# Optimization experiments

Hardware: AMD Instinct MI355X
Metric: run time of the kernel (lower is better)

## Reference

```python
import jax, jax.numpy as jnp
import numpy as np
from jax import lax

B_, DIM, H, W, Dd = 2, 256, 16, 16, 16
DI, N, DTR, K = 256, 8, 16, 4   # d_inner (expand=1), d_state, dt_rank=ceil(256/16), d_conv
OUT_C = 1200
L = H * W * Dd
EPS = 1e-5


def setup_inputs() -> dict:
    key = jax.random.key(0)
    ks = jax.random.split(key, 20)
    g = lambda k, s: jax.random.normal(k, s, jnp.float32) * 0.02
    A_log = jnp.log(jnp.broadcast_to(jnp.arange(1, N + 1, dtype=jnp.float32), (DI, N)))
    dt_bias = jnp.full((DI,), float(np.log(np.expm1(0.01))), jnp.float32)
    return {
        "input0": jax.random.normal(ks[0], (B_, DIM, H, W, Dd), jnp.float32),
        "input1": jax.random.normal(ks[1], (B_, DIM, H, W, Dd), jnp.float32),
        "norm0_w": jnp.ones((DIM,), jnp.float32),
        "norm0_b": jnp.zeros((DIM,), jnp.float32),
        "norm1_w": jnp.ones((DIM,), jnp.float32),
        "norm1_b": jnp.zeros((DIM,), jnp.float32),
        "in_proj_w": g(ks[2], (DI, DIM)),
        "in_projz_w": g(ks[3], (DI, DIM)),
        "conv1d_w": g(ks[4], (DI, 1, K)),
        "conv1d_bias": jnp.zeros((DI,), jnp.float32),
        "conv1db_w": g(ks[5], (DI, 1, K)),
        "conv1db_bias": jnp.zeros((DI,), jnp.float32),
        "xproj_w": g(ks[6], (DTR + 2 * N, DI)),
        "xprojb_w": g(ks[7], (DTR + 2 * N, DI)),
        "dtproj_w": g(ks[8], (DI, DTR)),
        "dtproj_bias": dt_bias,
        "dtprojb_w": g(ks[9], (DI, DTR)),
        "dtprojb_bias": dt_bias,
        "A_log": A_log,
        "Ab_log": A_log,
        "D_p": jnp.ones((DI,), jnp.float32),
        "D_b": jnp.ones((DI,), jnp.float32),
        "rms_w": jnp.ones((DI,), jnp.float32),
        "out_proj_w": g(ks[10], (DIM, DI)),
        "conv3d_w": g(ks[11], (OUT_C, DIM)),
        "conv3d_bias": jnp.zeros((OUT_C,), jnp.float32),
    }


def _layernorm(x, w, b):
    m = x.mean(-1, keepdims=True)
    v = ((x - m) ** 2).mean(-1, keepdims=True)
    return (x - m) * lax.rsqrt(v + EPS) * w + b


def _rmsnorm(x, w):
    return x * lax.rsqrt((x * x).mean(-1, keepdims=True) + EPS) * w


def _ssm_dir(x, z, conv_w, conv_b, xproj_w, dtproj_w, dtproj_bias, A_log, Dp):
    # One direction of the bimamba-v2 selective scan. x, z: (b, L, d_inner)
    xt = x.transpose(0, 2, 1)  # (b, d, L)
    xc = lax.conv_general_dilated(xt, conv_w, (1,), [(K - 1, 0)], feature_group_count=DI)
    x = jax.nn.silu(xc + conv_b[None, :, None]).transpose(0, 2, 1)  # causal dw-conv + silu
    dbl = x @ xproj_w.T                                   # (b, L, dt_rank + 2n)
    dt, Bm, Cm = dbl[..., :DTR], dbl[..., DTR:DTR + N], dbl[..., DTR + N:]
    dt = jax.nn.softplus(dt @ dtproj_w.T + dtproj_bias)    # (b, L, d)
    A = -jnp.exp(A_log)                                    # (d, n)
    dA = jnp.exp(dt[..., None] * A)                        # (b, L, d, n)
    dBu = (dt * x)[..., None] * Bm[:, :, None, :]          # (b, L, d, n)

    def step(h, inp):
        dA_t, dBu_t, C_t = inp
        h = h * dA_t + dBu_t
        return h, jnp.einsum('bdn,bn->bd', h, C_t)

    h0 = jnp.zeros((x.shape[0], DI, N), x.dtype)
    _, ys = lax.scan(step, h0, (dA.transpose(1, 0, 2, 3), dBu.transpose(1, 0, 2, 3), Cm.transpose(1, 0, 2)))
    y = ys.transpose(1, 0, 2) + x * Dp                     # (b, L, d)
    return y * jax.nn.silu(z)                              # gate from the matching branch


def _forward(input0, input1, norm0_w, norm0_b, norm1_w, norm1_b, in_proj_w, in_projz_w,
             conv1d_w, conv1d_bias, conv1db_w, conv1db_bias, xproj_w, xprojb_w,
             dtproj_w, dtproj_bias, dtprojb_w, dtprojb_bias, A_log, Ab_log,
             D_p, D_b, rms_w, out_proj_w, conv3d_w, conv3d_bias):
    b = input0.shape[0]
    skip = input0
    seq0 = input0.transpose(0, 2, 3, 4, 1).reshape(b, L, DIM)  # b (h w d) c
    seq1 = input1.transpose(0, 2, 3, 4, 1).reshape(b, L, DIM)
    seq0 = _layernorm(seq0, norm0_w, norm0_b)
    seq1 = _layernorm(seq1, norm1_w, norm1_b)
    x = seq0 @ in_proj_w.T    # SSM input from input0
    z = seq1 @ in_projz_w.T   # gate from extra_emb (input1)
    y_f = _ssm_dir(x, z, conv1d_w, conv1d_bias, xproj_w, dtproj_w, dtproj_bias, A_log, D_p)
    y_b = _ssm_dir(x[:, ::-1], z[:, ::-1], conv1db_w, conv1db_bias, xprojb_w,
                   dtprojb_w, dtprojb_bias, Ab_log, D_b)[:, ::-1]

    def head(y):
        o = _rmsnorm(y, rms_w) @ out_proj_w.T              # use_norm=True, then out_proj
        o = o.reshape(b, H, W, Dd, DIM).transpose(0, 4, 1, 2, 3) + skip
        return jnp.einsum('bchwd,oc->bohwd', o, conv3d_w) + conv3d_bias[None, :, None, None, None]

    out = head((y_f + y_b) * 0.5)   # if_devide_out=True
    return out, head(y_f), head(y_b)


def reference(input0, input1, norm0_w, norm0_b, norm1_w, norm1_b, in_proj_w, in_projz_w,
              conv1d_w, conv1d_bias, conv1db_w, conv1db_bias, xproj_w, xprojb_w,
              dtproj_w, dtproj_bias, dtprojb_w, dtprojb_bias, A_log, Ab_log,
              D_p, D_b, rms_w, out_proj_w, conv3d_w, conv3d_bias):
    return _forward(input0, input1, norm0_w, norm0_b, norm1_w, norm1_b, in_proj_w, in_projz_w,
                    conv1d_w, conv1d_bias, conv1db_w, conv1db_bias, xproj_w, xprojb_w,
                    dtproj_w, dtproj_bias, dtprojb_w, dtprojb_bias, A_log, Ab_log,
                    D_p, D_b, rms_w, out_proj_w, conv3d_w, conv3d_bias)
```

## Files before the change

kernel.cpp:

```cpp
#include <hip/hip_runtime.h>
#include <cstdint>

#define NTOK 8192

typedef __attribute__((ext_vector_type(4))) float f32x4;
typedef __attribute__((ext_vector_type(8))) short s16x8;

__device__ __forceinline__ short f2bf(float f) {
  union { float f; unsigned u; } x; x.f = f;
  unsigned r = x.u + 0x7FFFu + ((x.u >> 16) & 1u);
  return (short)(r >> 16);
}
__device__ __forceinline__ float bf2f(short s) {
  union { float f; unsigned u; } x;
  x.u = ((unsigned)(unsigned short)s) << 16;
  return x.f;
}
__device__ __forceinline__ void gl_lds16(const void* g, void* l) {
  __builtin_amdgcn_global_load_lds((const unsigned int*)g, (unsigned int*)l, 16, 0, 0);
}

__global__ __launch_bounds__(256) void ln_transpose_kernel(
    const float* __restrict__ in0, const float* __restrict__ in1,
    const float* __restrict__ w0, const float* __restrict__ b0,
    const float* __restrict__ w1, const float* __restrict__ b1,
    const float* __restrict__ wxp, const float* __restrict__ wzp,
    const float* __restrict__ wop, const float* __restrict__ wcp,
    short* __restrict__ Wx, short* __restrict__ Wz,
    short* __restrict__ Wo, short* __restrict__ Wc,
    short* __restrict__ xlnz, float* __restrict__ seqT)
{
  __shared__ float tile[32 * 257];
  __shared__ float mu[32], rs[32];
  const int tid = threadIdx.x;
  const int b  = blockIdx.x >> 7;
  const int l0 = (blockIdx.x & 127) << 5;

  {
    int base = (int)blockIdx.x << 11;
    #pragma unroll
    for (int i = 0; i < 8; ++i) {
      int idx = base + (i << 8) + tid;
      if (idx < 65536)       Wx[idx] = f2bf(wxp[idx]);
      else if (idx < 131072) Wz[idx - 65536] = f2bf(wzp[idx - 65536]);
      else if (idx < 196608) Wo[idx - 131072] = f2bf(wop[idx - 131072]);
      else {
        int k = idx - 196608;
        Wc[k] = ((k >> 8) < 1200) ? f2bf(wcp[k]) : (short)0;
      }
    }
  }

  for (int pass = 0; pass < 2; ++pass) {
    const float* in = pass ? in1 : in0;
    #pragma unroll 8
    for (int i = 0; i < 32; ++i) {
      int e = (i << 8) + tid;
      int c = e >> 5, lo = e & 31;
      tile[lo * 257 + c] = in[((size_t)(b * 256 + c) << 12) + l0 + lo];
    }
    __syncthreads();
    if (tid < 64) {
      int r = tid & 31, h = tid >> 5;
      float s = 0.f, ss = 0.f;
      #pragma unroll 16
      for (int c = h * 128; c < h * 128 + 128; ++c) {
        float v = tile[r * 257 + c];
        s += v; ss += v * v;
      }
      s  += __shfl_xor(s, 32, 64);
      ss += __shfl_xor(ss, 32, 64);
      if (h == 0) {
        float m = s * (1.f / 256.f);
        mu[r] = m;
        rs[r] = rsqrtf(ss * (1.f / 256.f) - m * m + 1e-5f);
      }
    }
    __syncthreads();
    const float* w  = pass ? w1 : w0;
    const float* bb = pass ? b1 : b0;
    float wv = w[tid], bv = bb[tid];
    #pragma unroll 8
    for (int i = 0; i < 32; ++i) {
      float v = tile[i * 257 + tid];
      int row = (pass ? 8192 : 0) + (b << 12) + l0 + i;
      xlnz[(size_t)row * 256 + tid] = f2bf((v - mu[i]) * rs[i] * wv + bv);
      if (pass == 0) seqT[(((size_t)b << 12) + l0 + i) * 256 + tid] = v;
    }
    __syncthreads();
  }
}

template <int EPI>
__global__ __launch_bounds__(256) void gemm_fast(
    const short* __restrict__ A, const short* __restrict__ W0,
    const short* __restrict__ W1, float* __restrict__ Cf,
    short* __restrict__ Cb, const float* __restrict__ ADD,
    const float* __restrict__ bias, int Msplit)
{
  __shared__ short As[4096];
  __shared__ short Bs[4096];
  const int tid  = threadIdx.x;
  const int lane = tid & 63, wave = tid >> 6;
  const int m0 = blockIdx.y << 7;
  const int n0 = blockIdx.x << 7;
  const short* W = (EPI == 0 && m0 >= Msplit) ? W1 : W0;

  const int sr = tid >> 2;
  const int sc = (tid & 3) << 3;
  const int mf = lane & 15, kq = lane >> 4;
  const int wm = (wave & 1) << 6, wn = (wave >> 1) << 6;

  const short* Ar0 = A + (size_t)(m0 + sr) * 256 + sc;
  const short* Ar1 = A + (size_t)(m0 + 64 + sr) * 256 + sc;
  const short* Br0 = W + (size_t)(n0 + sr) * 256 + sc;
  const short* Br1 = W + (size_t)(n0 + 64 + sr) * 256 + sc;
  short* AsW = &As[wave << 9];
  short* BsW = &Bs[wave << 9];

  f32x4 acc[4][4] = {};

  for (int kt = 0; kt < 256; kt += 32) {
    gl_lds16(Ar0 + kt, AsW);
    gl_lds16(Ar1 + kt, AsW + 2048);
    gl_lds16(Br0 + kt, BsW);
    gl_lds16(Br1 + kt, BsW + 2048);
    __syncthreads();
    s16x8 af[4], bfr[4];
    #pragma unroll
    for (int i = 0; i < 4; ++i)
      af[i] = *(const s16x8*)&As[((wm + (i << 4) + mf) << 5) + (kq << 3)];
    #pragma unroll
    for (int j = 0; j < 4; ++j)
      bfr[j] = *(const s16x8*)&Bs[((wn + (j << 4) + mf) << 5) + (kq << 3)];
    #pragma unroll
    for (int i = 0; i < 4; ++i)
      #pragma unroll
      for (int j = 0; j < 4; ++j)
        acc[i][j] = __builtin_amdgcn_mfma_f32_16x16x32_bf16(af[i], bfr[j], acc[i][j], 0, 0, 0);
    __syncthreads();
  }

  if (EPI == 0) {
    #pragma unroll
    for (int i = 0; i < 4; ++i) {
      int gm = m0 + wm + (i << 4) + (kq << 2);
      #pragma unroll
      for (int j = 0; j < 4; ++j) {
        int gn = n0 + wn + (j << 4) + mf;
        #pragma unroll
        for (int r = 0; r < 4; ++r)
          Cf[(size_t)(gm + r) * 256 + gn] = acc[i][j][r];
      }
    }
  } else if (EPI == 1) {
    #pragma unroll
    for (int i = 0; i < 4; ++i) {
      int gm = m0 + wm + (i << 4) + (kq << 2);
      #pragma unroll
      for (int j = 0; j < 4; ++j) {
        int gn = n0 + wn + (j << 4) + mf;
        #pragma unroll
        for (int r = 0; r < 4; ++r) {
          int tok = (gm + r) & 8191;
          float v = acc[i][j][r] + ADD[(size_t)tok * 256 + gn];
          Cb[(size_t)(gm + r) * 256 + gn] = f2bf(v);
        }
      }
    }
  } else {
    const int head = m0 >> 13, bb = (m0 >> 12) & 1, lb = m0 & 4095;
    float* obase = Cf + (size_t)head * (2u * 1200u * 4096u) + (size_t)bb * (1200u * 4096u);
    #pragma unroll
    for (int i = 0; i < 4; ++i) {
      int l = lb + wm + (i << 4) + (kq << 2);
      #pragma unroll
      for (int j = 0; j < 4; ++j) {
        int gn = n0 + wn + (j << 4) + mf;
        if (gn < 1200) {
          float bv = bias[gn];
          f32x4 v = acc[i][j];
          v[0] += bv; v[1] += bv; v[2] += bv; v[3] += bv;
          __builtin_nontemporal_store(v, (f32x4*)&obase[(size_t)gn * 4096 + l]);
        }
      }
    }
  }
}

__global__ __launch_bounds__(256) void fused_front(
    const float* __restrict__ x,
    const float* __restrict__ cw0, const float* __restrict__ cb0,
    const float* __restrict__ cw1, const float* __restrict__ cb1,
    const float* __restrict__ xw0, const float* __restrict__ xw1,
    const float* __restrict__ dtw0, const float* __restrict__ dtb0,
    const float* __restrict__ dtw1, const float* __restrict__ dtb1,
    const float* __restrict__ Alog0, const float* __restrict__ Alog1,
    float* __restrict__ xcg, float* __restrict__ dblg,
    float* __restrict__ P, float* __restrict__ Q)
{
  __shared__ float xcs[16 * 256];
  __shared__ short wxs[256 * 33];
  __shared__ float dls[512];
  const int tid = threadIdx.x;
  const int dir = blockIdx.x >> 9;
  const int b   = (blockIdx.x >> 8) & 1;
  const int ch  = blockIdx.x & 255;
  const int t0  = ch << 4;
  const float* cw   = dir ? cw1 : cw0;
  const float* cb   = dir ? cb1 : cb0;
  const float* xw   = dir ? xw1 : xw0;
  const float* dtw  = dir ? dtw1 : dtw0;
  const float* dtb  = dir ? dtb1 : dtb0;
  const float* Alog = dir ? Alog1 : Alog0;
  const size_t dS = (size_t)dir * (NTOK * 256);
  const size_t xb = ((size_t)b) << 12;

  {
    const int d = tid;
    const float w0 = cw[(d << 2)], w1 = cw[(d << 2) + 1],
                w2 = cw[(d << 2) + 2], w3 = cw[(d << 2) + 3];
    const float bias = cb[d];
    float h0 = 0.f, h1 = 0.f, h2 = 0.f;
    #pragma unroll
    for (int i = 0; i < 3; ++i) {
      int ts = t0 - 3 + i; float v = 0.f;
      if (ts >= 0) { int tn = dir ? 4095 - ts : ts; v = x[(xb + tn) * 256 + d]; }
      h0 = h1; h1 = h2; h2 = v;
    }
    #pragma unroll
    for (int s = 0; s < 16; ++s) {
      int ts = t0 + s;
      int tn = dir ? 4095 - ts : ts;
      float xv = x[(xb + tn) * 256 + d];
      float a = bias + w0 * h0 + w1 * h1 + w2 * h2 + w3 * xv;
      h0 = h1; h1 = h2; h2 = xv;
      float v = a / (1.f + __expf(-a));
      xcs[s * 256 + d] = v;
      xcg[dS + (xb + ts) * 256 + d] = v;
    }
  }
  #pragma unroll
  for (int i = 0; i < 32; ++i) {
    int flat = (i << 8) + tid;
    wxs[(flat & 255) * 33 + (flat >> 8)] = f2bf(xw[flat]);
  }
  __syncthreads();

  {
    const int j = tid & 31, s0 = tid >> 5;
    float a0 = 0.f, a1 = 0.f;
    #pragma unroll 8
    for (int r = 0; r < 256; ++r) {
      float w = bf2f(wxs[r * 33 + j]);
      a0 = fmaf(xcs[s0 * 256 + r], w, a0);
      a1 = fmaf(xcs[(s0 + 8) * 256 + r], w, a1);
    }
    dls[(s0 << 5) + j] = a0;
    dls[((s0 + 8) << 5) + j] = a1;
    size_t db = (size_t)dir * 262144 + ((xb + t0) << 5);
    dblg[db + tid] = a0;
    dblg[db + 256 + tid] = a1;
  }
  __syncthreads();

  {
    const int d = tid;
    float wrow[16];
    #pragma unroll
    for (int r = 0; r < 16; ++r) wrow[r] = dtw[(d << 4) + r];
    const float bias = dtb[d];
    float Av[8], p[8], q[8];
    #pragma unroll
    for (int n = 0; n < 8; ++n) {
      Av[n] = -expf(Alog[(d << 3) + n]); p[n] = 1.f; q[n] = 0.f;
    }
    for (int s = 0; s < 16; ++s) {
      float a = bias;
      #pragma unroll
      for (int r = 0; r < 16; ++r) a = fmaf(dls[(s << 5) + r], wrow[r], a);
      float dtv = (a > 20.f) ? a : log1pf(__expf(a));
      float xv = xcs[s * 256 + d];
      float du = dtv * xv;
      #pragma unroll
      for (int n = 0; n < 8; ++n) {
        float dA = __expf(dtv * Av[n]);
        p[n] *= dA;
        q[n] = fmaf(q[n], dA, du * dls[(s << 5) + 16 + n]);
      }
    }
    size_t ob = (size_t)dir * 1048576 + ((size_t)((b << 8) + ch) * 8) * 256 + d;
    #pragma unroll
    for (int n = 0; n < 8; ++n) { P[ob + (n << 8)] = p[n]; Q[ob + (n << 8)] = q[n]; }
  }
}

__global__ __launch_bounds__(256) void scan_p2(
    const float* __restrict__ P, const float* __restrict__ Q, float* __restrict__ Hs)
{
  const int d = threadIdx.x;
  const int bid = blockIdx.x;
  const int dir = bid >> 4, b = (bid >> 3) & 1, n = bid & 7;
  const size_t dOff = (size_t)dir * 1048576;
  float h = 0.f;
  #pragma unroll 8
  for (int ch = 0; ch < 256; ++ch) {
    size_t i = dOff + ((size_t)((b << 8) + ch) * 8 + n) * 256 + d;
    Hs[i] = h;
    h = fmaf(P[i], h, Q[i]);
  }
}

__global__ __launch_bounds__(256) void scan_p3(
    const float* __restrict__ xcg, const float* __restrict__ dblg,
    const float* __restrict__ dtw0, const float* __restrict__ dtb0,
    const float* __restrict__ dtw1, const float* __restrict__ dtb1,
    const float* __restrict__ Hs, const float* __restrict__ z,
    const float* __restrict__ Alog0, const float* __restrict__ Alog1,
    const float* __restrict__ Dp0, const float* __restrict__ Dp1,
    short* __restrict__ yall)
{
  __shared__ float dl[512];
  const int d = threadIdx.x;
  const int dir = blockIdx.x >> 9;
  const int b   = (blockIdx.x >> 8) & 1;
  const int ch  = blockIdx.x & 255;
  const int t0  = ch << 4;
  const float* dtw  = dir ? dtw1 : dtw0;
  const float* dtb  = dir ? dtb1 : dtb0;
  const float* Alog = dir ? Alog1 : Alog0;
  const float* Dp   = dir ? Dp1 : Dp0;
  const size_t dS = (size_t)dir * (NTOK * 256);
  const size_t xb = ((size_t)b) << 12;
  short* y = yall + (size_t)dir * (NTOK * 256);

  size_t db = (size_t)dir * 262144 + ((xb + t0) << 5);
  dl[d]       = dblg[db + d];
  dl[256 + d] = dblg[db + 256 + d];
  float wrow[16];
  #pragma unroll
  for (int r = 0; r < 16; ++r) wrow[r] = dtw[(d << 4) + r];
  const float bias = dtb[d];
  float Av[8], h[8];
  #pragma unroll
  for (int n = 0; n < 8; ++n) Av[n] = -expf(Alog[(d << 3) + n]);
  size_t hb = (size_t)dir * 1048576 + ((size_t)((b << 8) + ch) * 8) * 256 + d;
  #pragma unroll
  for (int n = 0; n < 8; ++n) h[n] = Hs[hb + (n << 8)];
  const float Dv = Dp[d];
  __syncthreads();
  for (int s = 0; s < 16; ++s) {
    float a = bias;
    #pragma unroll
    for (int r = 0; r < 16; ++r) a = fmaf(dl[(s << 5) + r], wrow[r], a);
    float dtv = (a > 20.f) ? a : log1pf(__expf(a));
    int ts = t0 + s;
    float xv = xcg[dS + (xb + ts) * 256 + d];
    float du = dtv * xv;
    float yv = 0.f;
    #pragma unroll
    for (int n = 0; n < 8; ++n) {
      float dA = __expf(dtv * Av[n]);
      h[n] = fmaf(h[n], dA, du * dl[(s << 5) + 16 + n]);
      yv = fmaf(h[n], dl[(s << 5) + 24 + n], yv);
    }
    yv = fmaf(xv, Dv, yv);
    int tn = dir ? (4095 - ts) : ts;
    size_t zi = (xb + tn) * 256 + d;
    float zv = z[zi];
    y[zi] = f2bf(yv * zv / (1.f + __expf(-zv)));
  }
}

__global__ __launch_bounds__(256) void rms_all(
    const short* __restrict__ yf, const short* __restrict__ yb,
    const float* __restrict__ w, short* __restrict__ yn)
{
  const int d = threadIdx.x;
  const int mode = blockIdx.y;
  const size_t tok = blockIdx.x;
  size_t i = tok * 256 + d;
  float v;
  if (mode == 0)      v = 0.5f * (bf2f(yf[i]) + bf2f(yb[i]));
  else if (mode == 1) v = bf2f(yf[i]);
  else                v = bf2f(yb[i]);
  float ss = v * v;
  #pragma unroll
  for (int o = 32; o > 0; o >>= 1) ss += __shfl_xor(ss, o, 64);
  __shared__ float red[4];
  if ((d & 63) == 0) red[d >> 6] = ss;
  __syncthreads();
  float tot = red[0] + red[1] + red[2] + red[3];
  float sc = rsqrtf(tot * (1.f / 256.f) + 1e-5f);
  yn[((size_t)mode * 8192 + tok) * 256 + d] = f2bf(v * sc * w[d]);
}

extern "C" void kernel_launch(void* const* d_in, const int* in_sizes, int n_in,
                              void* d_out, int out_size, void* d_ws, size_t ws_size,
                              hipStream_t stream) {
  const float* in0        = (const float*)d_in[0];
  const float* in1        = (const float*)d_in[1];
  const float* n0w        = (const float*)d_in[2];
  const float* n0b        = (const float*)d_in[3];
  const float* n1w        = (const float*)d_in[4];
  const float* n1b        = (const float*)d_in[5];
  const float* in_proj_w  = (const float*)d_in[6];
  const float* in_projz_w = (const float*)d_in[7];
  const float* conv1d_w   = (const float*)d_in[8];
  const float* conv1d_b   = (const float*)d_in[9];
  const float* conv1db_w  = (const float*)d_in[10];
  const float* conv1db_b  = (const float*)d_in[11];
  const float* xproj_w    = (const float*)d_in[12];
  const float* xprojb_w   = (const float*)d_in[13];
  const float* dtproj_w   = (const float*)d_in[14];
  const float* dtproj_b   = (const float*)d_in[15];
  const float* dtprojb_w  = (const float*)d_in[16];
  const float* dtprojb_b  = (const float*)d_in[17];
  const float* A_log      = (const float*)d_in[18];
  const float* Ab_log     = (const float*)d_in[19];
  const float* D_p        = (const float*)d_in[20];
  const float* D_b        = (const float*)d_in[21];
  const float* rms_w      = (const float*)d_in[22];
  const float* out_proj_w = (const float*)d_in[23];
  const float* conv3d_w   = (const float*)d_in[24];
  const float* conv3d_b   = (const float*)d_in[25];
  (void)in_sizes; (void)n_in; (void)out_size; (void)ws_size;

  float* ws = (float*)d_ws;
  size_t o = 0;
  short* xlnz = (short*)(ws + o); o += 2097152;
  float* seqT = ws + o;           o += 2097152;
  float* x    = ws + o;           o += 2097152;
  float* z    = ws + o;           o += 2097152;
  float* xc2  = ws + o;           o += 4194304;
  float* dbl2 = ws + o;           o += 524288;
  float* P    = ws + o;           o += 2097152;
  float* Q    = ws + o;           o += 2097152;
  float* Hs   = ws + o;           o += 2097152;
  short* yall = (short*)(ws + o); o += 2097152;
  short* yn   = (short*)(ws + o); o += 3145728;
  short* obuf = (short*)(ws + o); o += 3145728;
  short* Wx   = (short*)(ws + o); o += 32768;
  short* Wz   = (short*)(ws + o); o += 32768;
  short* Wo   = (short*)(ws + o); o += 32768;
  short* Wc   = (short*)(ws + o); o += 163840;
  float* out  = (float*)d_out;

  dim3 blk(256);

  ln_transpose_kernel<<<dim3(256), blk, 0, stream>>>(
      in0, in1, n0w, n0b, n1w, n1b,
      in_proj_w, in_projz_w, out_proj_w, conv3d_w, Wx, Wz, Wo, Wc,
      xlnz, seqT);

  gemm_fast<0><<<dim3(2, 128), blk, 0, stream>>>(xlnz, Wx, Wz, x, nullptr, nullptr, nullptr, 8192);

  fused_front<<<dim3(1024), blk, 0, stream>>>(
      x, conv1d_w, conv1d_b, conv1db_w, conv1db_b,
      xproj_w, xprojb_w, dtproj_w, dtproj_b, dtprojb_w, dtprojb_b,
      A_log, Ab_log, xc2, dbl2, P, Q);

  scan_p2<<<dim3(32), blk, 0, stream>>>(P, Q, Hs);

  scan_p3<<<dim3(1024), blk, 0, stream>>>(
      xc2, dbl2, dtproj_w, dtproj_b, dtprojb_w, dtprojb_b,
      Hs, z, A_log, Ab_log, D_p, D_b, yall);

  rms_all<<<dim3(8192, 3), blk, 0, stream>>>(yall, yall + 2097152, rms_w, yn);
  gemm_fast<1><<<dim3(2, 192), blk, 0, stream>>>(yn, Wo, nullptr, nullptr, obuf, seqT, nullptr, 0);
  gemm_fast<2><<<dim3(10, 192), blk, 0, stream>>>(obuf, Wc, nullptr, out, nullptr, nullptr, conv3d_b, 0);
}
```

Before: 339.0 us.

## Split SSM front into conv, MFMA x_proj GEMM, and hierarchical chunk scan

Replaces the fused_front kernel, which did the x_proj projection as a scalar LDS dot product per block, with three stages. A bf16 conv+SiLU kernel is followed by a small MFMA GEMM for the 32-wide x_proj output, with the weights pre-converted to bf16 in the setup kernel. The conv+SiLU is recomputed in scan_p1 and scan_p3 instead of storing and reloading fp32 xc, and those kernels read dbl straight from global memory. The serial 256-step inter-chunk scan (32 blocks) becomes a two-level scan over 512 blocks each, adding launches and redundant conv work in exchange for more parallelism and tensor-core use.

```diff
diff --git a/kernel.cpp b/kernel.cpp
--- a/kernel.cpp
+++ b/kernel.cpp
@@ -26,8 +26,9 @@
     const float* __restrict__ w1, const float* __restrict__ b1,
     const float* __restrict__ wxp, const float* __restrict__ wzp,
     const float* __restrict__ wop, const float* __restrict__ wcp,
+    const float* __restrict__ xwf, const float* __restrict__ xwb,
     short* __restrict__ Wx, short* __restrict__ Wz,
-    short* __restrict__ Wo, short* __restrict__ Wc,
+    short* __restrict__ Wo, short* __restrict__ Wc, short* __restrict__ Wxp,
     short* __restrict__ xlnz, float* __restrict__ seqT)
 {
   __shared__ float tile[32 * 257];
@@ -36,18 +37,17 @@
   const int b  = blockIdx.x >> 7;
   const int l0 = (blockIdx.x & 127) << 5;
 
-  {
-    int base = (int)blockIdx.x << 11;
-    #pragma unroll
-    for (int i = 0; i < 8; ++i) {
-      int idx = base + (i << 8) + tid;
-      if (idx < 65536)       Wx[idx] = f2bf(wxp[idx]);
-      else if (idx < 131072) Wz[idx - 65536] = f2bf(wzp[idx - 65536]);
-      else if (idx < 196608) Wo[idx - 131072] = f2bf(wop[idx - 131072]);
-      else {
-        int k = idx - 196608;
-        Wc[k] = ((k >> 8) < 1200) ? f2bf(wcp[k]) : (short)0;
-      }
+  for (int idx = (int)blockIdx.x * 256 + tid; idx < 540672; idx += 65536) {
+    if (idx < 65536)       Wx[idx] = f2bf(wxp[idx]);
+    else if (idx < 131072) Wz[idx - 65536] = f2bf(wzp[idx - 65536]);
+    else if (idx < 196608) Wo[idx - 131072] = f2bf(wop[idx - 131072]);
+    else if (idx < 524288) {
+      int k = idx - 196608;
+      Wc[k] = ((k >> 8) < 1200) ? f2bf(wcp[k]) : (short)0;
+    } else {
+      int k = idx - 524288;
+      int j = k & 8191;
+      Wxp[k] = f2bf((k >> 13) ? xwb[j] : xwf[j]);
     }
   }
 
@@ -188,36 +188,91 @@
   }
 }
 
-__global__ __launch_bounds__(256) void fused_front(
+__global__ __launch_bounds__(256) void conv_silu_b(
     const float* __restrict__ x,
     const float* __restrict__ cw0, const float* __restrict__ cb0,
     const float* __restrict__ cw1, const float* __restrict__ cb1,
-    const float* __restrict__ xw0, const float* __restrict__ xw1,
+    short* __restrict__ xcb)
+{
+  const int d = threadIdx.x;
+  const int dir = blockIdx.x >> 9;
+  const int b   = (blockIdx.x >> 8) & 1;
+  const int t0  = (blockIdx.x & 255) << 4;
+  const float* cw = dir ? cw1 : cw0;
+  const float* cb = dir ? cb1 : cb0;
+  const float w0 = cw[(d << 2)], w1 = cw[(d << 2) + 1],
+              w2 = cw[(d << 2) + 2], w3 = cw[(d << 2) + 3];
+  const float bias = cb[d];
+  const size_t xb = ((size_t)b) << 12;
+  short* orow = xcb + ((size_t)(dir << 13) + (b << 12) + t0) * 256 + d;
+  float h0 = 0.f, h1 = 0.f, h2 = 0.f;
+  #pragma unroll
+  for (int i = 0; i < 3; ++i) {
+    int ts = t0 - 3 + i; float v = 0.f;
+    if (ts >= 0) { int tn = dir ? 4095 - ts : ts; v = x[(xb + tn) * 256 + d]; }
+    h0 = h1; h1 = h2; h2 = v;
+  }
+  #pragma unroll
+  for (int s = 0; s < 16; ++s) {
+    int tn = dir ? 4095 - (t0 + s) : (t0 + s);
+    float xv = x[(xb + tn) * 256 + d];
+    float a = bias + w0 * h0 + w1 * h1 + w2 * h2 + w3 * xv;
+    h0 = h1; h1 = h2; h2 = xv;
+    orow[(size_t)s * 256] = f2bf(a / (1.f + __expf(-a)));
+  }
+}
+
+__global__ __launch_bounds__(256) void gemm_n32(
+    const short* __restrict__ A, const short* __restrict__ Wxp,
+    float* __restrict__ Cdbl)
+{
+  const int lane = threadIdx.x & 63, wave = threadIdx.x >> 6;
+  const int mf = lane & 15, kq = lane >> 4;
+  const int m0 = ((int)blockIdx.x << 6) + (wave << 4);
+  const short* W = Wxp + ((m0 >= 8192) ? 8192 : 0);
+  const short* Arow = A + (size_t)(m0 + mf) * 256 + (kq << 3);
+  const short* B0 = W + (size_t)mf * 256 + (kq << 3);
+  const short* B1 = W + (size_t)(16 + mf) * 256 + (kq << 3);
+  f32x4 acc[2] = {};
+  #pragma unroll
+  for (int kt = 0; kt < 256; kt += 32) {
+    s16x8 af = *(const s16x8*)(Arow + kt);
+    s16x8 b0 = *(const s16x8*)(B0 + kt);
+    s16x8 b1 = *(const s16x8*)(B1 + kt);
+    acc[0] = __builtin_amdgcn_mfma_f32_16x16x32_bf16(af, b0, acc[0], 0, 0, 0);
+    acc[1] = __builtin_amdgcn_mfma_f32_16x16x32_bf16(af, b1, acc[1], 0, 0, 0);
+  }
+  #pragma unroll
+  for (int j = 0; j < 2; ++j)
+    #pragma unroll
+    for (int r = 0; r < 4; ++r)
+      Cdbl[(size_t)(m0 + (kq << 2) + r) * 32 + (j << 4) + mf] = acc[j][r];
+}
+
+__global__ __launch_bounds__(256) void scan_p1(
+    const float* __restrict__ x,
+    const float* __restrict__ cw0, const float* __restrict__ cb0,
+    const float* __restrict__ cw1, const float* __restrict__ cb1,
+    const float* __restrict__ dbl,
     const float* __restrict__ dtw0, const float* __restrict__ dtb0,
     const float* __restrict__ dtw1, const float* __restrict__ dtb1,
-    const float* __restrict__ Alog0, const float* __restrict__ Alog1,
-    float* __restrict__ xcg, float* __restrict__ dblg,
+    const float* __restrict__ Al0, const float* __restrict__ Al1,
     float* __restrict__ P, float* __restrict__ Q)
 {
-  __shared__ float xcs[16 * 256];
-  __shared__ short wxs[256 * 33];
-  __shared__ float dls[512];
-  const int tid = threadIdx.x;
+  const int d = threadIdx.x;
   const int dir = blockIdx.x >> 9;
   const int b   = (blockIdx.x >> 8) & 1;
   const int ch  = blockIdx.x & 255;
   const int t0  = ch << 4;
   const float* cw   = dir ? cw1 : cw0;
   const float* cb   = dir ? cb1 : cb0;
-  const float* xw   = dir ? xw1 : xw0;
   const float* dtw  = dir ? dtw1 : dtw0;
   const float* dtb  = dir ? dtb1 : dtb0;
-  const float* Alog = dir ? Alog1 : Alog0;
-  const size_t dS = (size_t)dir * (NTOK * 256);
+  const float* Alog = dir ? Al1 : Al0;
   const size_t xb = ((size_t)b) << 12;
 
+  float xc[16];
   {
-    const int d = tid;
     const float w0 = cw[(d << 2)], w1 = cw[(d << 2) + 1],
                 w2 = cw[(d << 2) + 2], w3 = cw[(d << 2) + 3];
     const float bias = cb[d];
@@ -230,141 +285,162 @@
     }
     #pragma unroll
     for (int s = 0; s < 16; ++s) {
-      int ts = t0 + s;
-      int tn = dir ? 4095 - ts : ts;
+      int tn = dir ? 4095 - (t0 + s) : (t0 + s);
       float xv = x[(xb + tn) * 256 + d];
       float a = bias + w0 * h0 + w1 * h1 + w2 * h2 + w3 * xv;
       h0 = h1; h1 = h2; h2 = xv;
-      float v = a / (1.f + __expf(-a));
-      xcs[s * 256 + d] = v;
-      xcg[dS + (xb + ts) * 256 + d] = v;
-    }
-  }
-  #pragma unroll
-  for (int i = 0; i < 32; ++i) {
-    int flat = (i << 8) + tid;
-    wxs[(flat & 255) * 33 + (flat >> 8)] = f2bf(xw[flat]);
-  }
-  __syncthreads();
-
-  {
-    const int j = tid & 31, s0 = tid >> 5;
-    float a0 = 0.f, a1 = 0.f;
-    #pragma unroll 8
-    for (int r = 0; r < 256; ++r) {
-      float w = bf2f(wxs[r * 33 + j]);
-      a0 = fmaf(xcs[s0 * 256 + r], w, a0);
-      a1 = fmaf(xcs[(s0 + 8) * 256 + r], w, a1);
-    }
-    dls[(s0 << 5) + j] = a0;
-    dls[((s0 + 8) << 5) + j] = a1;
-    size_t db = (size_t)dir * 262144 + ((xb + t0) << 5);
-    dblg[db + tid] = a0;
-    dblg[db + 256 + tid] = a1;
-  }
-  __syncthreads();
-
-  {
-    const int d = tid;
-    float wrow[16];
-    #pragma unroll
-    for (int r = 0; r < 16; ++r) wrow[r] = dtw[(d << 4) + r];
-    const float bias = dtb[d];
-    float Av[8], p[8], q[8];
+      xc[s] = a / (1.f + __expf(-a));
+    }
+  }
+
+  float wrow[16];
+  #pragma unroll
+  for (int r = 0; r < 16; ++r) wrow[r] = dtw[(d << 4) + r];
+  const float bias_dt = dtb[d];
+  float Av[8], p[8], q[8];
+  #pragma unroll
+  for (int n = 0; n < 8; ++n) {
+    Av[n] = -expf(Alog[(d << 3) + n]); p[n] = 1.f; q[n] = 0.f;
+  }
+  const float* drow = dbl + ((size_t)(dir << 13) + (b << 12) + t0) * 32;
+  #pragma unroll 4
+  for (int s = 0; s < 16; ++s) {
+    float a = bias_dt;
+    #pragma unroll
+    for (int r = 0; r < 16; ++r) a = fmaf(drow[(s << 5) + r], wrow[r], a);
+    float dtv = (a > 20.f) ? a : log1pf(__expf(a));
+    float du = dtv * xc[s];
     #pragma unroll
     for (int n = 0; n < 8; ++n) {
-      Av[n] = -expf(Alog[(d << 3) + n]); p[n] = 1.f; q[n] = 0.f;
-    }
-    for (int s = 0; s < 16; ++s) {
-      float a = bias;
-      #pragma unroll
-      for (int r = 0; r < 16; ++r) a = fmaf(dls[(s << 5) + r], wrow[r], a);
-      float dtv = (a > 20.f) ? a : log1pf(__expf(a));
-      float xv = xcs[s * 256 + d];
-      float du = dtv * xv;
-      #pragma unroll
-      for (int n = 0; n < 8; ++n) {
-        float dA = __expf(dtv * Av[n]);
-        p[n] *= dA;
-        q[n] = fmaf(q[n], dA, du * dls[(s << 5) + 16 + n]);
-      }
-    }
-    size_t ob = (size_t)dir * 1048576 + ((size_t)((b << 8) + ch) * 8) * 256 + d;
-    #pragma unroll
-    for (int n = 0; n < 8; ++n) { P[ob + (n << 8)] = p[n]; Q[ob + (n << 8)] = q[n]; }
-  }
-}
-
-__global__ __launch_bounds__(256) void scan_p2(
-    const float* __restrict__ P, const float* __restrict__ Q, float* __restrict__ Hs)
+      float dA = __expf(dtv * Av[n]);
+      p[n] *= dA;
+      q[n] = fmaf(q[n], dA, du * drow[(s << 5) + 16 + n]);
+    }
+  }
+  size_t ob = (size_t)dir * 1048576 + ((size_t)((b << 8) + ch) << 11) + d;
+  #pragma unroll
+  for (int n = 0; n < 8; ++n) { P[ob + (n << 8)] = p[n]; Q[ob + (n << 8)] = q[n]; }
+}
+
+__global__ __launch_bounds__(256) void scan_p2a(
+    const float* __restrict__ P, const float* __restrict__ Q,
+    float* __restrict__ SP, float* __restrict__ SQ)
 {
   const int d = threadIdx.x;
   const int bid = blockIdx.x;
-  const int dir = bid >> 4, b = (bid >> 3) & 1, n = bid & 7;
-  const size_t dOff = (size_t)dir * 1048576;
+  const int dir = bid >> 8, b = (bid >> 7) & 1, n = (bid >> 4) & 7, sup = bid & 15;
+  float sp = 1.f, sq = 0.f;
+  #pragma unroll 4
+  for (int c = 0; c < 16; ++c) {
+    int ch = (sup << 4) + c;
+    size_t i = (size_t)dir * 1048576 + ((size_t)((b << 8) + ch) << 11) + (n << 8) + d;
+    float pp = P[i], qq = Q[i];
+    sq = fmaf(pp, sq, qq);
+    sp *= pp;
+  }
+  size_t o2 = ((size_t)((((dir << 1) + b) << 3) + n) << 12) + ((size_t)sup << 8) + d;
+  SP[o2] = sp; SQ[o2] = sq;
+}
+
+__global__ __launch_bounds__(256) void scan_p2bc(
+    const float* __restrict__ P, const float* __restrict__ Q,
+    const float* __restrict__ SP, const float* __restrict__ SQ,
+    float* __restrict__ Hs)
+{
+  const int d = threadIdx.x;
+  const int bid = blockIdx.x;
+  const int dir = bid >> 8, b = (bid >> 7) & 1, n = (bid >> 4) & 7, sup = bid & 15;
+  size_t sb = ((size_t)((((dir << 1) + b) << 3) + n) << 12) + d;
   float h = 0.f;
-  #pragma unroll 8
-  for (int ch = 0; ch < 256; ++ch) {
-    size_t i = dOff + ((size_t)((b << 8) + ch) * 8 + n) * 256 + d;
+  for (int s2 = 0; s2 < sup; ++s2) {
+    size_t i = sb + ((size_t)s2 << 8);
+    h = fmaf(SP[i], h, SQ[i]);
+  }
+  #pragma unroll 4
+  for (int c = 0; c < 16; ++c) {
+    int ch = (sup << 4) + c;
+    size_t i = (size_t)dir * 1048576 + ((size_t)((b << 8) + ch) << 11) + (n << 8) + d;
     Hs[i] = h;
     h = fmaf(P[i], h, Q[i]);
   }
 }
 
 __global__ __launch_bounds__(256) void scan_p3(
-    const float* __restrict__ xcg, const float* __restrict__ dblg,
+    const float* __restrict__ x,
+    const float* __restrict__ cw0, const float* __restrict__ cb0,
+    const float* __restrict__ cw1, const float* __restrict__ cb1,
+    const float* __restrict__ dbl,
     const float* __restrict__ dtw0, const float* __restrict__ dtb0,
     const float* __restrict__ dtw1, const float* __restrict__ dtb1,
     const float* __restrict__ Hs, const float* __restrict__ z,
-    const float* __restrict__ Alog0, const float* __restrict__ Alog1,
+    const float* __restrict__ Al0, const float* __restrict__ Al1,
     const float* __restrict__ Dp0, const float* __restrict__ Dp1,
     short* __restrict__ yall)
 {
-  __shared__ float dl[512];
   const int d = threadIdx.x;
   const int dir = blockIdx.x >> 9;
   const int b   = (blockIdx.x >> 8) & 1;
   const int ch  = blockIdx.x & 255;
   const int t0  = ch << 4;
+  const float* cw   = dir ? cw1 : cw0;
+  const float* cb   = dir ? cb1 : cb0;
   const float* dtw  = dir ? dtw1 : dtw0;
   const float* dtb  = dir ? dtb1 : dtb0;
-  const float* Alog = dir ? Alog1 : Alog0;
+  const float* Alog = dir ? Al1 : Al0;
   const float* Dp   = dir ? Dp1 : Dp0;
-  const size_t dS = (size_t)dir * (NTOK * 256);
   const size_t xb = ((size_t)b) << 12;
   short* y = yall + (size_t)dir * (NTOK * 256);
 
-  size_t db = (size_t)dir * 262144 + ((xb + t0) << 5);
-  dl[d]       = dblg[db + d];
-  dl[256 + d] = dblg[db + 256 + d];
+  float xc[16];
+  {
+    const float w0 = cw[(d << 2)], w1 = cw[(d << 2) + 1],
+                w2 = cw[(d << 2) + 2], w3 = cw[(d << 2) + 3];
+    const float bias = cb[d];
+    float h0 = 0.f, h1 = 0.f, h2 = 0.f;
+    #pragma unroll
+    for (int i = 0; i < 3; ++i) {
+      int ts = t0 - 3 + i; float v = 0.f;
+      if (ts >= 0) { int tn = dir ? 4095 - ts : ts; v = x[(xb + tn) * 256 + d]; }
+      h0 = h1; h1 = h2; h2 = v;
+    }
+    #pragma unroll
+    for (int s = 0; s < 16; ++s) {
+      int tn = dir ? 4095 - (t0 + s) : (t0 + s);
+      float xv = x[(xb + tn) * 256 + d];
+      float a = bias + w0 * h0 + w1 * h1 + w2 * h2 + w3 * xv;
+      h0 = h1; h1 = h2; h2 = xv;
+      xc[s] = a / (1.f + __expf(-a));
+    }
+  }
+
   float wrow[16];
   #pragma unroll
   for (int r = 0; r < 16; ++r) wrow[r] = dtw[(d << 4) + r];
-  const float bias = dtb[d];
+  const float bias_dt = dtb[d];
   float Av[8], h[8];
   #pragma unroll
   for (int n = 0; n < 8; ++n) Av[n] = -expf(Alog[(d << 3) + n]);
-  size_t hb = (size_t)dir * 1048576 + ((size_t)((b << 8) + ch) * 8) * 256 + d;
+  size_t hb = (size_t)dir * 1048576 + ((size_t)((b << 8) + ch) << 11) + d;
   #pragma unroll
   for (int n = 0; n < 8; ++n) h[n] = Hs[hb + (n << 8)];
   const float Dv = Dp[d];
-  __syncthreads();
+  const float* drow = dbl + ((size_t)(dir << 13) + (b << 12) + t0) * 32;
+  #pragma unroll 4
   for (int s = 0; s < 16; ++s) {
-    float a = bias;
-    #pragma unroll
-    for (int r = 0; r < 16; ++r) a = fmaf(dl[(s << 5) + r], wrow[r], a);
+    float a = bias_dt;
+    #pragma unroll
+    for (int r = 0; r < 16; ++r) a = fmaf(drow[(s << 5) + r], wrow[r], a);
     float dtv = (a > 20.f) ? a : log1pf(__expf(a));
-    int ts = t0 + s;
-    float xv = xcg[dS + (xb + ts) * 256 + d];
-    float du = dtv * xv;
+    float du = dtv * xc[s];
     float yv = 0.f;
     #pragma unroll
     for (int n = 0; n < 8; ++n) {
       float dA = __expf(dtv * Av[n]);
-      h[n] = fmaf(h[n], dA, du * dl[(s << 5) + 16 + n]);
-      yv = fmaf(h[n], dl[(s << 5) + 24 + n], yv);
-    }
-    yv = fmaf(xv, Dv, yv);
+      h[n] = fmaf(h[n], dA, du * drow[(s << 5) + 16 + n]);
+      yv = fmaf(h[n], drow[(s << 5) + 24 + n], yv);
+    }
+    yv = fmaf(xc[s], Dv, yv);
+    int ts = t0 + s;
     int tn = dir ? (4095 - ts) : ts;
     size_t zi = (xb + tn) * 256 + d;
     float zv = z[zi];
@@ -432,11 +508,13 @@
   float* seqT = ws + o;           o += 2097152;
   float* x    = ws + o;           o += 2097152;
   float* z    = ws + o;           o += 2097152;
-  float* xc2  = ws + o;           o += 4194304;
-  float* dbl2 = ws + o;           o += 524288;
+  short* xcb  = (short*)(ws + o); o += 2097152;
+  float* dbl  = ws + o;           o += 524288;
   float* P    = ws + o;           o += 2097152;
   float* Q    = ws + o;           o += 2097152;
   float* Hs   = ws + o;           o += 2097152;
+  float* SP   = ws + o;           o += 131072;
+  float* SQ   = ws + o;           o += 131072;
   short* yall = (short*)(ws + o); o += 2097152;
   short* yn   = (short*)(ws + o); o += 3145728;
   short* obuf = (short*)(ws + o); o += 3145728;
@@ -444,27 +522,33 @@
   short* Wz   = (short*)(ws + o); o += 32768;
   short* Wo   = (short*)(ws + o); o += 32768;
   short* Wc   = (short*)(ws + o); o += 163840;
+  short* Wxp  = (short*)(ws + o); o += 8192;
   float* out  = (float*)d_out;
 
   dim3 blk(256);
 
   ln_transpose_kernel<<<dim3(256), blk, 0, stream>>>(
       in0, in1, n0w, n0b, n1w, n1b,
-      in_proj_w, in_projz_w, out_proj_w, conv3d_w, Wx, Wz, Wo, Wc,
-      xlnz, seqT);
+      in_proj_w, in_projz_w, out_proj_w, conv3d_w, xproj_w, xprojb_w,
+      Wx, Wz, Wo, Wc, Wxp, xlnz, seqT);
 
   gemm_fast<0><<<dim3(2, 128), blk, 0, stream>>>(xlnz, Wx, Wz, x, nullptr, nullptr, nullptr, 8192);
 
-  fused_front<<<dim3(1024), blk, 0, stream>>>(
-      x, conv1d_w, conv1d_b, conv1db_w, conv1db_b,
-      xproj_w, xprojb_w, dtproj_w, dtproj_b, dtprojb_w, dtprojb_b,
-      A_log, Ab_log, xc2, dbl2, P, Q);
-
-  scan_p2<<<dim3(32), blk, 0, stream>>>(P, Q, Hs);
+  conv_silu_b<<<dim3(1024), blk, 0, stream>>>(x, conv1d_w, conv1d_b, conv1db_w, conv1db_b, xcb);
+
+  gemm_n32<<<dim3(256), blk, 0, stream>>>(xcb, Wxp, dbl);
+
+  scan_p1<<<dim3(1024), blk, 0, stream>>>(
+      x, conv1d_w, conv1d_b, conv1db_w, conv1db_b, dbl,
+      dtproj_w, dtproj_b, dtprojb_w, dtprojb_b, A_log, Ab_log, P, Q);
+
+  scan_p2a<<<dim3(512), blk, 0, stream>>>(P, Q, SP, SQ);
+  scan_p2bc<<<dim3(512), blk, 0, stream>>>(P, Q, SP, SQ, Hs);
 
   scan_p3<<<dim3(1024), blk, 0, stream>>>(
-      xc2, dbl2, dtproj_w, dtproj_b, dtprojb_w, dtprojb_b,
-      Hs, z, A_log, Ab_log, D_p, D_b, yall);
+      x, conv1d_w, conv1d_b, conv1db_w, conv1db_b, dbl,
+      dtproj_w, dtproj_b, dtprojb_w, dtprojb_b, Hs, z,
+      A_log, Ab_log, D_p, D_b, yall);
 
   rms_all<<<dim3(8192, 3), blk, 0, stream>>>(yall, yall + 2097152, rms_w, yn);
   gemm_fast<1><<<dim3(2, 192), blk, 0, stream>>>(yn, Wo, nullptr, nullptr, obuf, seqT, nullptr, 0);
```

New measurement: 339.6 us. Within noise of the previous version (+0.2%).
